# Kernel optimization log

Measured on AMD Instinct MI355X. Metric: run time of the kernel, lower is better.

Reference implementation:

```python
import jax, jax.numpy as jnp
import numpy as np

L = 8      # subsequence_len
A = 4      # alphabet_size
D = 256    # sketch_dim
SEQ = 16384


def setup_inputs() -> dict:
    key = jax.random.key(0)
    k1, k2, k3 = jax.random.split(key, 3)
    sequence = jax.random.randint(k1, (SEQ,), 0, A)
    # stacked nn.Embedding weights: (L, A, D), init N(0, 0.5)
    hash_emb = 0.5 * jax.random.normal(k2, (L, A, D), dtype=jnp.float32)
    sign_logits = 0.5 * jax.random.normal(k3, (L, A), dtype=jnp.float32)
    return {"sequence": sequence, "hash_emb": hash_emb, "sign_logits": sign_logits}


def _forward(sequence, hash_emb, sign_logits):
    # roll_idx[j, s] = (j - s) % D  so that gather reproduces torch.roll(t, s)[j] = t[(j - s) % D]
    roll_idx = (jnp.arange(D)[:, None] - jnp.arange(D)[None, :]) % D
    p_arr = jnp.arange(1, L + 1, dtype=jnp.float32)           # p = 1..L
    Tp0 = jnp.zeros((L + 1, D), dtype=jnp.float32).at[0, 0].set(1.0)
    Tm0 = jnp.zeros((L + 1, D), dtype=jnp.float32)

    def step(carry, xs):
        Tp, Tm = carry                                         # (L+1, D) each
        c, i = xs
        valid = (c >= 0) & (c < A)
        c_safe = jnp.clip(c, 0, A - 1)
        # eval-mode soft hash: softmax over the embedding row (per level p)
        probs = jax.nn.softmax(hash_emb[:, c_safe, :], axis=-1)   # (L, D)
        sign = jax.nn.sigmoid(sign_logits[:, c_safe])             # (L,)
        denom = (i + 1).astype(jnp.float32)
        # z = p/(i+1); levels with p > i+1 (and invalid chars) are frozen (z=0)
        z = jnp.where((p_arr <= denom) & valid, p_arr / denom, 0.0)  # (L,)
        Tp_prev, Tm_prev = Tp[:L], Tm[:L]                         # (L, D)
        # expected circular shift: out[l, j] = sum_s probs[l, s] * T_prev[l, (j-s)%D]
        stp = jnp.einsum('ljs,ls->lj', Tp_prev[:, roll_idx], probs)
        stm = jnp.einsum('ljs,ls->lj', Tm_prev[:, roll_idx], probs)
        s = sign[:, None]
        upd_p = s * stp + (1.0 - s) * stm
        upd_m = s * stm + (1.0 - s) * stp
        zc = z[:, None]
        new_Tp = Tp.at[1:].set((1.0 - zc) * Tp[1:] + zc * upd_p)
        new_Tm = Tm.at[1:].set((1.0 - zc) * Tm[1:] + zc * upd_m)
        return (new_Tp, new_Tm), None

    step = jax.checkpoint(step)
    (Tp, Tm), _ = jax.lax.scan(step, (Tp0, Tm0), (sequence, jnp.arange(SEQ)))
    return Tp[L] - Tm[L]


def reference(sequence, hash_emb, sign_logits):
    return _forward(sequence, hash_emb, sign_logits)
```

## Files before the change

kernel.cpp:

```cpp
#include <hip/hip_runtime.h>
#include <math.h>

#define LL 8
#define AA 4
#define DD 256
#define KF 129
#define KH 128
#define CLEN 64
#define NCH 256
#define NES 36
#define LPAD 37

typedef float v2f __attribute__((ext_vector_type(2)));

#define SIX(l2,l1) ((((l2)*((l2)-1))>>1) + (l1))
#define SLOT(s)    ((s)*LPAD + ((s)>>1))

#define Q_OFF   0
#define V_OFF   (32*KF*2)
#define CNT_OFF (V_OFF + 2*KF)

__device__ __forceinline__ float invCN8() {
  constexpr double c = (16384.0 * 16383.0 * 16382.0 * 16381.0 *
                        16380.0 * 16379.0 * 16378.0 * 16377.0) / 40320.0;
  return (float)(1.0 / c);
}

__device__ __forceinline__ v2f cfma(const v2f b, const v2f a, v2f acc) {
  const v2f bb = (v2f){ b.x,  b.x};
  const v2f bw = (v2f){-b.y,  b.y};
  const v2f as = (v2f){ a.y,  a.x};
  acc = __builtin_elementwise_fma(bb, a,  acc);
  acc = __builtin_elementwise_fma(bw, as, acc);
  return acc;
}

template <unsigned MASK>
__device__ __forceinline__ void prodCols(const v2f* __restrict__ A, const v2f* __restrict__ B,
                                         v2f (&o)[NES]) {
#pragma unroll
  for (int l1 = 0; l1 < 8; ++l1) {
    if ((MASK >> l1) & 1) {
#pragma unroll
      for (int l2 = l1 + 1; l2 <= 8; ++l2) {
        v2f acc = A[SIX(l2, l1)] + B[SIX(l2, l1)];
#pragma unroll
        for (int m = l1 + 1; m < l2; ++m) acc = cfma(B[SIX(l2, m)], A[SIX(m, l1)], acc);
        o[SIX(l2, l1)] = acc;
      }
    }
  }
}

template <unsigned MASK>
__device__ __forceinline__ void writeCols(v2f* __restrict__ D, const v2f (&o)[NES]) {
#pragma unroll
  for (int l1 = 0; l1 < 8; ++l1) {
    if ((MASK >> l1) & 1) {
#pragma unroll
      for (int l2 = l1 + 1; l2 <= 8; ++l2) D[SIX(l2, l1)] = o[SIX(l2, l1)];
    }
  }
}

__device__ __forceinline__ void prodFullRA(const v2f (&A)[NES], const v2f* __restrict__ B,
                                           v2f (&o)[NES]) {
#pragma unroll
  for (int l1 = 0; l1 < 8; ++l1) {
#pragma unroll
    for (int l2 = l1 + 1; l2 <= 8; ++l2) {
      v2f acc = A[SIX(l2, l1)] + B[SIX(l2, l1)];
#pragma unroll
      for (int m = l1 + 1; m < l2; ++m) acc = cfma(B[SIX(l2, m)], A[SIX(m, l1)], acc);
      o[SIX(l2, l1)] = acc;
    }
  }
}

__device__ __forceinline__ void prodR(const float* __restrict__ A, const float* __restrict__ B,
                                      float (&o)[NES]) {
#pragma unroll
  for (int l1 = 0; l1 < 8; ++l1) {
#pragma unroll
    for (int l2 = l1 + 1; l2 <= 8; ++l2) {
      float acc = A[SIX(l2, l1)] + B[SIX(l2, l1)];
#pragma unroll
      for (int m = l1 + 1; m < l2; ++m) acc = fmaf(B[SIX(l2, m)], A[SIX(m, l1)], acc);
      o[SIX(l2, l1)] = acc;
    }
  }
}

__global__ __launch_bounds__(256) void kq(const float* __restrict__ hemb,
                                          const float* __restrict__ slog,
                                          float* __restrict__ Q,
                                          int* __restrict__ cnt) {
  const int b = blockIdx.x;
  const int t = threadIdx.x;
  if (b == 0 && t == 0)
    __hip_atomic_store(&cnt[0], 0, __ATOMIC_RELEASE, __HIP_MEMORY_SCOPE_AGENT);
  __shared__ float sh[DD];
  __shared__ float red[256];
  __shared__ float2 tw[256];
  {
    float sn, cs;
    __sincosf((float)t * (-0.0245436926061702596754894014319f), &sn, &cs);
    tw[t] = make_float2(cs, sn);
  }
  float h = hemb[b * DD + t];
  red[t] = h; __syncthreads();
  for (int off = 128; off > 0; off >>= 1) {
    if (t < off) red[t] = fmaxf(red[t], red[t + off]);
    __syncthreads();
  }
  float mx = red[0]; __syncthreads();
  float e = expf(h - mx);
  red[t] = e; __syncthreads();
  for (int off = 128; off > 0; off >>= 1) {
    if (t < off) red[t] += red[t + off];
    __syncthreads();
  }
  float s = red[0];
  sh[t] = e / s;
  __syncthreads();
  if (t < KF) {
    float cr = 0.0f, ci = 0.0f;
    for (int j = 0; j < DD; ++j) {
      const int m = (t * j) & 255;
      const float2 w = tw[m];
      const float p = sh[j];
      cr = fmaf(p, w.x, cr);
      ci = fmaf(p, w.y, ci);
    }
    const float sl = slog[b];
    const float sg = 1.0f / (1.0f + expf(-sl));
    const float q = fmaf(2.0f, sg, -1.0f);
    Q[(b * KF + t) * 2 + 0] = q * cr;
    Q[(b * KF + t) * 2 + 1] = q * ci;
  }
}

__global__ __launch_bounds__(256, 1) void kmain(const int* __restrict__ seq,
                                                const float* __restrict__ Q,
                                                float* __restrict__ v,
                                                int* __restrict__ cnt,
                                                float* __restrict__ outp) {
  const int blk = blockIdx.x;
  const int t   = threadIdx.x;
  __shared__ __align__(16) float ldsf[9600];
  __shared__ __align__(16) float4 qtab[LL * AA];

  if (blk < KH) {
    const int k = blk;
    const float2* Q2 = (const float2*)Q;
    if (t < LL * AA) {
      const float2 q = Q2[t * KF + k];
      qtab[t] = make_float4(q.x, q.x, -q.y, q.y);
    }
    __syncthreads();

    v2f G[NES];
#pragma unroll
    for (int e = 0; e < NES; ++e) G[e] = (v2f){0.f, 0.f};

    const int4* sp = (const int4*)(seq + t * CLEN);
    for (int sb = 0; sb < CLEN / 4; ++sb) {
      const int4 cs = sp[sb];
      const int csy[4] = {cs.x, cs.y, cs.z, cs.w};
#pragma unroll
      for (int u = 0; u < 4; ++u) {
        const int c = csy[u];
        float4 qv[LL];
#pragma unroll
        for (int l = 0; l < LL; ++l) qv[l] = qtab[(l << 2) | c];
#pragma unroll
        for (int l = LL; l >= 1; --l) {
          const float4 q4 = qv[l - 1];
          const v2f qa = (v2f){q4.x, q4.y};
          const v2f qb = (v2f){q4.z, q4.w};
          {
            v2f g = G[SIX(l, l - 1)];
            g.x += q4.x; g.y += q4.w;
            G[SIX(l, l - 1)] = g;
          }
#pragma unroll
          for (int l1 = 0; l1 < l - 1; ++l1) {
            const v2f H  = G[SIX(l - 1, l1)];
            const v2f Hs = (v2f){H.y, H.x};
            v2f g = G[SIX(l, l1)];
            g = __builtin_elementwise_fma(qa, H,  g);
            g = __builtin_elementwise_fma(qb, Hs, g);
            G[SIX(l, l1)] = g;
          }
        }
      }
    }

    v2f* L = (v2f*)ldsf;
    if (t & 1) {
      v2f* D = L + SLOT(t >> 1);
#pragma unroll
      for (int e = 0; e < NES; ++e) D[e] = G[e];
    }
    __syncthreads();
    if (!(t & 1)) {
      v2f o[NES];
      prodFullRA(G, L + SLOT(t >> 1), o);
      v2f* D = L + SLOT(t >> 1);
#pragma unroll
      for (int e = 0; e < NES; ++e) D[e] = o[e];
    }
    __syncthreads();

    const int w = t >> 6;
    const int j = t & 63;
    v2f pc[NES];
    for (int n = 64; n >= 8; n >>= 1) {
      const bool act = (j < n);
      if (act) {
        const v2f* Ab = L + SLOT(2 * j);
        const v2f* Bb = L + SLOT(2 * j + 1);
        switch (w) {
          case 0:  prodCols<0x01>(Ab, Bb, pc); break;
          case 1:  prodCols<0x42>(Ab, Bb, pc); break;
          case 2:  prodCols<0x14>(Ab, Bb, pc); break;
          default: prodCols<0xA8>(Ab, Bb, pc); break;
        }
      }
      __syncthreads();
      if (act) {
        v2f* Db = L + SLOT(j);
        switch (w) {
          case 0:  writeCols<0x01>(Db, pc); break;
          case 1:  writeCols<0x42>(Db, pc); break;
          case 2:  writeCols<0x14>(Db, pc); break;
          default: writeCols<0xA8>(Db, pc); break;
        }
      }
      __syncthreads();
    }

    if (t < 64) {
      v2f sv[LL + 1];
      sv[0] = (v2f){1.f, 0.f};
#pragma unroll
      for (int l = 1; l <= LL; ++l) sv[l] = (v2f){0.f, 0.f};
      for (int gg = 0; gg < 8; ++gg) {
        v2f nv = (v2f){0.f, 0.f};
        if (t >= 1 && t <= LL) {
          nv = sv[t];
          const v2f* Bb = L + SLOT(gg);
          const int rb = (t * (t - 1)) >> 1;
#pragma unroll
          for (int l1 = 0; l1 < 8; ++l1) {
            if (l1 < t) nv = cfma(Bb[rb + l1], sv[l1], nv);
          }
        }
#pragma unroll
        for (int l = 1; l <= LL; ++l) {
          sv[l].x = __shfl(nv.x, l);
          sv[l].y = __shfl(nv.y, l);
        }
      }
      if (t == 0) {
        __hip_atomic_store(&v[2 * k],     sv[LL].x, __ATOMIC_RELEASE, __HIP_MEMORY_SCOPE_AGENT);
        __hip_atomic_store(&v[2 * k + 1], sv[LL].y, __ATOMIC_RELEASE, __HIP_MEMORY_SCOPE_AGENT);
      }
    }
  } else {
    float* Lr = ldsf;
    float Q8[LL][AA];
#pragma unroll
    for (int lc = 0; lc < LL * AA; ++lc) Q8[lc >> 2][lc & 3] = Q[(lc * KF + KH) * 2];

    float Gr[NES];
#pragma unroll
    for (int e = 0; e < NES; ++e) Gr[e] = 0.f;

    const int4* sp = (const int4*)(seq + t * CLEN);
    for (int sb = 0; sb < CLEN / 4; ++sb) {
      const int4 cs = sp[sb];
      const int csy[4] = {cs.x, cs.y, cs.z, cs.w};
#pragma unroll
      for (int u = 0; u < 4; ++u) {
        const int c = csy[u];
        float Qs[LL];
#pragma unroll
        for (int l = 0; l < LL; ++l) {
          const float qa = (c & 1) ? Q8[l][1] : Q8[l][0];
          const float qb = (c & 1) ? Q8[l][3] : Q8[l][2];
          Qs[l] = (c & 2) ? qb : qa;
        }
#pragma unroll
        for (int l = LL; l >= 1; --l) {
          Gr[SIX(l, l - 1)] += Qs[l - 1];
#pragma unroll
          for (int l1 = 0; l1 < l - 1; ++l1)
            Gr[SIX(l, l1)] = fmaf(Qs[l - 1], Gr[SIX(l - 1, l1)], Gr[SIX(l, l1)]);
        }
      }
    }
#pragma unroll
    for (int e = 0; e < NES; ++e) Lr[t * LPAD + e] = Gr[e];
    __syncthreads();

    float po[NES];
    for (int n = 128; n >= 1; n >>= 1) {
      const bool act = (t < n);
      if (act) prodR(Lr + (2 * t) * LPAD, Lr + (2 * t + 1) * LPAD, po);
      __syncthreads();
      if (act) { for (int e = 0; e < NES; ++e) Lr[t * LPAD + e] = po[e]; }
      __syncthreads();
    }
    if (t == 0) {
      __hip_atomic_store(&v[2 * KH],     Lr[SIX(LL, 0)], __ATOMIC_RELEASE, __HIP_MEMORY_SCOPE_AGENT);
      __hip_atomic_store(&v[2 * KH + 1], 0.0f,           __ATOMIC_RELEASE, __HIP_MEMORY_SCOPE_AGENT);
    }
  }

  __shared__ int isLast;
  __syncthreads();
  if (t == 0) {
    const int old = __hip_atomic_fetch_add(&cnt[0], 1, __ATOMIC_ACQ_REL, __HIP_MEMORY_SCOPE_AGENT);
    isLast = (old == KH) ? 1 : 0;
  }
  __syncthreads();
  if (isLast) {
    __shared__ float2 twd[256];
    __shared__ float dvr[KF], dvi[KF];
    {
      float sn, cs;
      __sincosf((float)t * 0.0245436926061702596754894014319f, &sn, &cs);
      twd[t] = make_float2(cs, sn);
    }
    if (t < KF) {
      dvr[t] = __hip_atomic_load(&v[2 * t],     __ATOMIC_ACQUIRE, __HIP_MEMORY_SCOPE_AGENT);
      dvi[t] = __hip_atomic_load(&v[2 * t + 1], __ATOMIC_ACQUIRE, __HIP_MEMORY_SCOPE_AGENT);
    }
    if (t == 0) {
      __hip_atomic_store(&cnt[0], 0, __ATOMIC_RELEASE, __HIP_MEMORY_SCOPE_AGENT);
    }
    __syncthreads();
    const float sc = (1.0f / 256.0f) * invCN8();
    float sum = dvr[0] + ((t & 1) ? -dvr[KH] : dvr[KH]);
    for (int k2 = 1; k2 < KH; ++k2) {
      const int m = (t * k2) & 255;
      const float2 wv = twd[m];
      sum = fmaf(2.0f * dvr[k2], wv.x, sum);
      sum = fmaf(-2.0f * dvi[k2], wv.y, sum);
    }
    outp[t] = sum * sc;
  }
}

extern "C" void kernel_launch(void* const* d_in, const int* in_sizes, int n_in,
                              void* d_out, int out_size, void* d_ws, size_t ws_size,
                              hipStream_t stream) {
  (void)in_sizes; (void)n_in; (void)out_size; (void)ws_size;
  const int*   seq  = (const int*)d_in[0];
  const float* hemb = (const float*)d_in[1];
  const float* slog = (const float*)d_in[2];
  float* ws   = (float*)d_ws;
  float* Q    = ws + Q_OFF;
  float* v    = ws + V_OFF;
  int*   cnt  = (int*)(ws + CNT_OFF);
  float* o    = (float*)d_out;

  hipLaunchKernelGGL(kq,    dim3(LL * AA), dim3(256), 0, stream, hemb, slog, Q, cnt);
  hipLaunchKernelGGL(kmain, dim3(KF),      dim3(256), 0, stream, seq, Q, v, cnt, o);
}
```

Before: 98.46 us.

## Fuse softmax/DFT precompute kernel into main kernel per frequency block

Removes the separate kq kernel. Each main-kernel block now computes only the DFT coefficients it needs: 8 threads per (level, char) row do the softmax and a single-frequency DFT, with shuffle reductions, writing straight into LDS qtab. The counter reset moves to a hipMemsetAsync, and the twiddle table is built once up front and reused by the final inverse DFT. This drops a kernel launch and the global round trip for Q, at the cost of redundant exp work in each of the 129 blocks.

```diff
diff --git a/kernel.cpp b/kernel.cpp
--- a/kernel.cpp
+++ b/kernel.cpp
@@ -7,7 +7,6 @@
 #define KF 129
 #define KH 128
 #define CLEN 64
-#define NCH 256
 #define NES 36
 #define LPAD 37
 
@@ -16,9 +15,8 @@
 #define SIX(l2,l1) ((((l2)*((l2)-1))>>1) + (l1))
 #define SLOT(s)    ((s)*LPAD + ((s)>>1))
 
-#define Q_OFF   0
-#define V_OFF   (32*KF*2)
-#define CNT_OFF (V_OFF + 2*KF)
+#define V_OFF   0
+#define CNT_OFF (2 * KF)
 
 __device__ __forceinline__ float invCN8() {
   constexpr double c = (16384.0 * 16383.0 * 16382.0 * 16381.0 *
@@ -91,57 +89,9 @@
   }
 }
 
-__global__ __launch_bounds__(256) void kq(const float* __restrict__ hemb,
-                                          const float* __restrict__ slog,
-                                          float* __restrict__ Q,
-                                          int* __restrict__ cnt) {
-  const int b = blockIdx.x;
-  const int t = threadIdx.x;
-  if (b == 0 && t == 0)
-    __hip_atomic_store(&cnt[0], 0, __ATOMIC_RELEASE, __HIP_MEMORY_SCOPE_AGENT);
-  __shared__ float sh[DD];
-  __shared__ float red[256];
-  __shared__ float2 tw[256];
-  {
-    float sn, cs;
-    __sincosf((float)t * (-0.0245436926061702596754894014319f), &sn, &cs);
-    tw[t] = make_float2(cs, sn);
-  }
-  float h = hemb[b * DD + t];
-  red[t] = h; __syncthreads();
-  for (int off = 128; off > 0; off >>= 1) {
-    if (t < off) red[t] = fmaxf(red[t], red[t + off]);
-    __syncthreads();
-  }
-  float mx = red[0]; __syncthreads();
-  float e = expf(h - mx);
-  red[t] = e; __syncthreads();
-  for (int off = 128; off > 0; off >>= 1) {
-    if (t < off) red[t] += red[t + off];
-    __syncthreads();
-  }
-  float s = red[0];
-  sh[t] = e / s;
-  __syncthreads();
-  if (t < KF) {
-    float cr = 0.0f, ci = 0.0f;
-    for (int j = 0; j < DD; ++j) {
-      const int m = (t * j) & 255;
-      const float2 w = tw[m];
-      const float p = sh[j];
-      cr = fmaf(p, w.x, cr);
-      ci = fmaf(p, w.y, ci);
-    }
-    const float sl = slog[b];
-    const float sg = 1.0f / (1.0f + expf(-sl));
-    const float q = fmaf(2.0f, sg, -1.0f);
-    Q[(b * KF + t) * 2 + 0] = q * cr;
-    Q[(b * KF + t) * 2 + 1] = q * ci;
-  }
-}
-
 __global__ __launch_bounds__(256, 1) void kmain(const int* __restrict__ seq,
-                                                const float* __restrict__ Q,
+                                                const float* __restrict__ hemb,
+                                                const float* __restrict__ slog,
                                                 float* __restrict__ v,
                                                 int* __restrict__ cnt,
                                                 float* __restrict__ outp) {
@@ -149,15 +99,77 @@
   const int t   = threadIdx.x;
   __shared__ __align__(16) float ldsf[9600];
   __shared__ __align__(16) float4 qtab[LL * AA];
+  __shared__ float2 twd[256];
+  __shared__ float dvr[KF], dvi[KF];
+  __shared__ int isLast;
+
+  {
+    float sn, cs;
+    __sincosf((float)t * 0.0245436926061702596754894014319f, &sn, &cs);
+    twd[t] = make_float2(cs, sn);
+  }
+  __syncthreads();
+
+  {
+    const int r  = t >> 3;
+    const int g8 = t & 7;
+    float4 hv[8];
+#pragma unroll
+    for (int u = 0; u < 8; ++u)
+      hv[u] = *(const float4*)(hemb + r * DD + u * 32 + g8 * 4);
+    float mx = -1e30f;
+#pragma unroll
+    for (int u = 0; u < 8; ++u) {
+      mx = fmaxf(mx, fmaxf(fmaxf(hv[u].x, hv[u].y), fmaxf(hv[u].z, hv[u].w)));
+    }
+    mx = fmaxf(mx, __shfl_xor(mx, 1));
+    mx = fmaxf(mx, __shfl_xor(mx, 2));
+    mx = fmaxf(mx, __shfl_xor(mx, 4));
+
+    float sum = 0.0f, cr = 0.0f, ci = 0.0f;
+    if (blk < KH) {
+      const int k = blk;
+#pragma unroll
+      for (int u = 0; u < 8; ++u) {
+        const float ev[4] = {expf(hv[u].x - mx), expf(hv[u].y - mx),
+                             expf(hv[u].z - mx), expf(hv[u].w - mx)};
+#pragma unroll
+        for (int w = 0; w < 4; ++w) {
+          const int j = u * 32 + g8 * 4 + w;
+          const int m = (j * k) & 255;
+          const float2 tv = twd[m];
+          sum += ev[w];
+          cr = fmaf(ev[w], tv.x, cr);
+          ci = fmaf(-ev[w], tv.y, ci);
+        }
+      }
+    } else {
+#pragma unroll
+      for (int u = 0; u < 8; ++u) {
+        const float ev[4] = {expf(hv[u].x - mx), expf(hv[u].y - mx),
+                             expf(hv[u].z - mx), expf(hv[u].w - mx)};
+        sum += ev[0] + ev[1] + ev[2] + ev[3];
+        cr  += (ev[0] - ev[1]) + (ev[2] - ev[3]);
+      }
+    }
+    sum += __shfl_xor(sum, 1); cr += __shfl_xor(cr, 1); ci += __shfl_xor(ci, 1);
+    sum += __shfl_xor(sum, 2); cr += __shfl_xor(cr, 2); ci += __shfl_xor(ci, 2);
+    sum += __shfl_xor(sum, 4); cr += __shfl_xor(cr, 4); ci += __shfl_xor(ci, 4);
+
+    if (g8 == 0) {
+      const float sl = slog[r];
+      const float sg = 1.0f / (1.0f + expf(-sl));
+      const float q  = fmaf(2.0f, sg, -1.0f);
+      const float sc = q / sum;
+      const float qr = cr * sc;
+      const float qi = ci * sc;
+      qtab[r] = make_float4(qr, qr, -qi, qi);
+    }
+  }
+  __syncthreads();
 
   if (blk < KH) {
     const int k = blk;
-    const float2* Q2 = (const float2*)Q;
-    if (t < LL * AA) {
-      const float2 q = Q2[t * KF + k];
-      qtab[t] = make_float4(q.x, q.x, -q.y, q.y);
-    }
-    __syncthreads();
 
     v2f G[NES];
 #pragma unroll
@@ -271,7 +283,7 @@
     float* Lr = ldsf;
     float Q8[LL][AA];
 #pragma unroll
-    for (int lc = 0; lc < LL * AA; ++lc) Q8[lc >> 2][lc & 3] = Q[(lc * KF + KH) * 2];
+    for (int lc = 0; lc < LL * AA; ++lc) Q8[lc >> 2][lc & 3] = qtab[lc].x;
 
     float Gr[NES];
 #pragma unroll
@@ -318,7 +330,6 @@
     }
   }
 
-  __shared__ int isLast;
   __syncthreads();
   if (t == 0) {
     const int old = __hip_atomic_fetch_add(&cnt[0], 1, __ATOMIC_ACQ_REL, __HIP_MEMORY_SCOPE_AGENT);
@@ -326,13 +337,6 @@
   }
   __syncthreads();
   if (isLast) {
-    __shared__ float2 twd[256];
-    __shared__ float dvr[KF], dvi[KF];
-    {
-      float sn, cs;
-      __sincosf((float)t * 0.0245436926061702596754894014319f, &sn, &cs);
-      twd[t] = make_float2(cs, sn);
-    }
     if (t < KF) {
       dvr[t] = __hip_atomic_load(&v[2 * t],     __ATOMIC_ACQUIRE, __HIP_MEMORY_SCOPE_AGENT);
       dvi[t] = __hip_atomic_load(&v[2 * t + 1], __ATOMIC_ACQUIRE, __HIP_MEMORY_SCOPE_AGENT);
@@ -361,11 +365,10 @@
   const float* hemb = (const float*)d_in[1];
   const float* slog = (const float*)d_in[2];
   float* ws   = (float*)d_ws;
-  float* Q    = ws + Q_OFF;
   float* v    = ws + V_OFF;
   int*   cnt  = (int*)(ws + CNT_OFF);
   float* o    = (float*)d_out;
 
-  hipLaunchKernelGGL(kq,    dim3(LL * AA), dim3(256), 0, stream, hemb, slog, Q, cnt);
-  hipLaunchKernelGGL(kmain, dim3(KF),      dim3(256), 0, stream, seq, Q, v, cnt, o);
-}
+  hipMemsetAsync(cnt, 0, sizeof(int), stream);
+  hipLaunchKernelGGL(kmain, dim3(KF), dim3(256), 0, stream, seq, hemb, slog, v, cnt, o);
+}
```

Result: faster. 95.86 us (-2.6%).
